# Performance work log

Hardware: AMD Instinct MI355X
Metric: run time of the kernel (lower is better)

Reference implementation:

```python
import jax, jax.numpy as jnp
import numpy as np


def setup_inputs() -> dict:
    key = jax.random.key(0)
    k1, k2, k3, k4 = jax.random.split(key, 4)
    d_in, d_out = 1024, 1024
    x = jax.random.normal(k1, (4, 2048, d_in), dtype=jnp.float32)
    # nn.Linear weights, stored as [d_in, d_out] for x @ W (torch stores transpose)
    s = 1.0 / np.sqrt(d_in)
    Wq = jax.random.normal(k2, (d_in, d_out), dtype=jnp.float32) * s
    Wk = jax.random.normal(k3, (d_in, d_out), dtype=jnp.float32) * s
    Wv = jax.random.normal(k4, (d_in, d_out), dtype=jnp.float32) * s
    return {"x": x, "Wq": Wq, "Wk": Wk, "Wv": Wv}


def reference(x, Wq, Wk, Wv):
    # x: [b, s, d_in]; projections (no bias)
    q = jnp.einsum('bsi,io->bso', x, Wq)
    k = jnp.einsum('bsi,io->bso', x, Wk)
    v = jnp.einsum('bsi,io->bso', x, Wv)
    d_out = k.shape[-1]
    scores = jnp.einsum('bqd,bkd->bqk', q, k) / jnp.sqrt(jnp.float32(d_out))
    seq_len = x.shape[1]
    causal = jnp.tril(jnp.ones((seq_len, seq_len), dtype=bool))  # [s, s]
    scores = jnp.where(causal[None, :, :], scores, -jnp.inf)
    weights = jax.nn.softmax(scores, axis=-1)
    return jnp.einsum('bqk,bkd->bqd', weights, v)
```

## Files before the change

### kernel.cpp

```cpp
#include <hip/hip_runtime.h>

typedef __attribute__((ext_vector_type(8))) short bf16x8;
typedef __attribute__((ext_vector_type(4))) float f32x4;
typedef unsigned int u32;

__device__ __forceinline__ unsigned short f2bf(float f) {
  union { float f; unsigned int u; } a; a.f = f;
  unsigned int u = a.u;
  u += 0x7FFFu + ((u >> 16) & 1u);
  return (unsigned short)(u >> 16);
}

__device__ __forceinline__ void gload16(const unsigned short* g, unsigned short* l) {
  __builtin_amdgcn_global_load_lds((const __attribute__((address_space(1))) u32*)g,
                                   (__attribute__((address_space(3))) u32*)l, 16, 0, 0);
}

#define TM 128
#define TN 128
#define BK 64

template<int MODE>
__global__ __launch_bounds__(256, 4)
void gemm_bt(const unsigned short* __restrict__ A,
             const unsigned short* __restrict__ Bm,
             float* __restrict__ Cf,
             float* __restrict__ Cf2,
             unsigned short* __restrict__ Cb,
             int K, long aBatch, long bBatch, long cBatch, float scale)
{
  int z = blockIdx.z;
  A  += (long)z * aBatch;
  Bm += (long)z * bBatch;
  if (MODE == 2) { Cb += (long)z * cBatch; Cf += (long)z * 2048; }
  if (MODE == 3) { Cf += (long)z * cBatch; Cf2 += (long)z * 2048; }

  int bm, bn;
  if (MODE == 2) {
    int f = blockIdx.x;
    int r = (int)((sqrtf((float)(8 * f + 1)) - 1.0f) * 0.5f);
    while ((r + 1) * (r + 2) / 2 <= f) r++;
    while (r * (r + 1) / 2 > f) r--;
    bm = r * TM;
    bn = (f - r * (r + 1) / 2) * TN;
  } else if (MODE == 3) {
    bm = (15 - blockIdx.y) * TM;
    bn = blockIdx.x * TN;
  } else {
    bm = blockIdx.y * TM;
    bn = blockIdx.x * TN;
  }
  int Keff = (MODE == 3) ? (bm + TM) : K;

  __shared__ __align__(16) unsigned short As[TM * BK];
  __shared__ __align__(16) unsigned short Bs[TN * BK];

  int tid  = threadIdx.x;
  int wave = tid >> 6, lane = tid & 63;
  int wm = (wave >> 1) * 64, wn = (wave & 1) * 64;
  int quad = lane >> 4, l16 = lane & 15;

  int r8 = lane >> 3;
  int c  = (lane & 7) ^ r8;
  int rs = wave * 32 + r8;
  const unsigned short* Ag = A  + (long)(bm + rs) * K + c * 8;
  const unsigned short* Bg = Bm + (long)(bn + rs) * K + c * 8;
  unsigned short* Al = &As[(wave * 32) * BK];
  unsigned short* Bl = &Bs[(wave * 32) * BK];

  f32x4 acc[4][4] = {};

  for (int k0 = 0; k0 < Keff; k0 += BK) {
#pragma unroll
    for (int g = 0; g < 4; g++) {
      gload16(Ag + k0 + (long)g * 8 * K, Al + g * 8 * BK);
      gload16(Bg + k0 + (long)g * 8 * K, Bl + g * 8 * BK);
    }
    __syncthreads();

#pragma unroll
    for (int h = 0; h < 2; h++) {
      bf16x8 af[4], bfr[4];
#pragma unroll
      for (int i = 0; i < 4; i++)
        af[i]  = *(const bf16x8*)&As[(wm + i * 16 + l16) * BK + (((quad + 4 * h) ^ (l16 & 7)) * 8)];
#pragma unroll
      for (int j = 0; j < 4; j++)
        bfr[j] = *(const bf16x8*)&Bs[(wn + j * 16 + l16) * BK + (((quad + 4 * h) ^ (l16 & 7)) * 8)];
#pragma unroll
      for (int i = 0; i < 4; i++)
#pragma unroll
        for (int j = 0; j < 4; j++)
          acc[i][j] = __builtin_amdgcn_mfma_f32_16x16x32_bf16(af[i], bfr[j], acc[i][j], 0, 0, 0);
    }
    __syncthreads();
  }

#pragma unroll
  for (int i = 0; i < 4; i++) {
    int grow0 = bm + wm + i * 16 + quad * 4;
    if (MODE == 2) {
#pragma unroll
      for (int r = 0; r < 4; r++) {
        int grow = grow0 + r;
        float rowpart = 0.f;
#pragma unroll
        for (int j = 0; j < 4; j++) {
          int gcol = bn + wn + j * 16 + l16;
          float e = (gcol <= grow) ? __expf(acc[i][j][r] * scale) : 0.f;
          rowpart += e;
          Cb[(long)grow * 2048 + gcol] = f2bf(e);
        }
        rowpart += __shfl_xor(rowpart, 1);
        rowpart += __shfl_xor(rowpart, 2);
        rowpart += __shfl_xor(rowpart, 4);
        rowpart += __shfl_xor(rowpart, 8);
        if (l16 == 0) atomicAdd(&Cf[grow], rowpart);
      }
    } else if (MODE == 3) {
      float rinv[4];
#pragma unroll
      for (int r = 0; r < 4; r++) rinv[r] = 1.0f / Cf2[grow0 + r];
#pragma unroll
      for (int j = 0; j < 4; j++) {
        int gcol = bn + wn + j * 16 + l16;
#pragma unroll
        for (int r = 0; r < 4; r++)
          Cf[(long)(grow0 + r) * 1024 + gcol] = acc[i][j][r] * rinv[r];
      }
    } else {
#pragma unroll
      for (int j = 0; j < 4; j++) {
        int gcol = bn + wn + j * 16 + l16;
        int which = gcol >> 10;
        int col = gcol & 1023;
        if (which < 2) {
          unsigned short* dst = Cb + (long)which * 8192 * 1024;
#pragma unroll
          for (int r = 0; r < 4; r++)
            dst[(long)(grow0 + r) * 1024 + col] = f2bf(acc[i][j][r]);
        } else {
          unsigned short* Vt = Cb + (long)2 * 8192 * 1024;
          int bb = grow0 >> 11, s = grow0 & 2047;
          ushort4 pk;
          pk.x = f2bf(acc[i][j][0]); pk.y = f2bf(acc[i][j][1]);
          pk.z = f2bf(acc[i][j][2]); pk.w = f2bf(acc[i][j][3]);
          *(ushort4*)(Vt + ((long)bb * 1024 + col) * 2048 + s) = pk;
        }
      }
    }
  }
}

__global__ __launch_bounds__(256)
void cvt_bf16(const float* __restrict__ in, unsigned short* __restrict__ out, long n)
{
  long i = ((long)blockIdx.x * 256 + threadIdx.x) * 4;
  if (i >= n) return;
  float4 v = *(const float4*)(in + i);
  ushort4 o;
  o.x = f2bf(v.x); o.y = f2bf(v.y); o.z = f2bf(v.z); o.w = f2bf(v.w);
  *(ushort4*)(out + i) = o;
}

__global__ __launch_bounds__(256)
void zero_rsum(float* __restrict__ rsum)
{
  long i = ((long)blockIdx.x * 256 + threadIdx.x) * 4;
  float4 zz = {0.f, 0.f, 0.f, 0.f};
  *(float4*)(rsum + i) = zz;
}

__global__ __launch_bounds__(256)
void trans_cvt(const float* __restrict__ W0, const float* __restrict__ W1, const float* __restrict__ W2,
               unsigned short* __restrict__ T0, unsigned short* __restrict__ T1, unsigned short* __restrict__ T2)
{
  int z = blockIdx.z;
  const float* W   = (z == 0) ? W0 : (z == 1) ? W1 : W2;
  unsigned short* T = (z == 0) ? T0 : (z == 1) ? T1 : T2;
  __shared__ float tile[32][33];
  int kb = blockIdx.x * 32, nb = blockIdx.y * 32;
  int tx = threadIdx.x & 31, ty = threadIdx.x >> 5;
  for (int r = ty; r < 32; r += 8)
    tile[r][tx] = W[(long)(kb + r) * 1024 + nb + tx];
  __syncthreads();
  for (int r = ty; r < 32; r += 8)
    T[(long)(nb + r) * 1024 + kb + tx] = f2bf(tile[tx][r]);
}

extern "C" void kernel_launch(void* const* d_in, const int* in_sizes, int n_in,
                              void* d_out, int out_size, void* d_ws, size_t ws_size,
                              hipStream_t stream) {
  const float* x  = (const float*)d_in[0];
  const float* Wq = (const float*)d_in[1];
  const float* Wk = (const float*)d_in[2];
  const float* Wv = (const float*)d_in[3];
  float* out = (float*)d_out;

  unsigned short* Xb  = (unsigned short*)d_ws;
  unsigned short* WqT = Xb  + (long)8192 * 1024;
  unsigned short* Q   = WqT + (long)3072 * 1024;
  unsigned short* Kb  = Q   + (long)8192 * 1024;
  unsigned short* Vt  = Kb  + (long)8192 * 1024;
  unsigned short* E   = Vt  + (long)8192 * 1024;
  float* rsum         = (float*)(E + (long)4 * 2048 * 2048);
  unsigned short* WkT = WqT + (long)1024 * 1024;
  unsigned short* WvT = WkT + (long)1024 * 1024;

  cvt_bf16<<<8192, 256, 0, stream>>>(x, Xb, (long)8388608);
  trans_cvt<<<dim3(32, 32, 3), 256, 0, stream>>>(Wq, Wk, Wv, WqT, WkT, WvT);
  zero_rsum<<<8, 256, 0, stream>>>(rsum);

  gemm_bt<0><<<dim3(24, 64, 1), 256, 0, stream>>>(Xb, WqT, nullptr, nullptr, Q,
      1024, 0, 0, 0, 1.f);

  gemm_bt<2><<<dim3(136, 1, 4), 256, 0, stream>>>(Q, Kb, rsum, nullptr, E, 1024,
      (long)2048 * 1024, (long)2048 * 1024, (long)2048 * 2048, 0.03125f);

  gemm_bt<3><<<dim3(8, 16, 4), 256, 0, stream>>>(E, Vt, out, rsum, nullptr, 2048,
      (long)2048 * 2048, (long)1024 * 2048, (long)2048 * 1024, 1.f);
}
```

Baseline: 239.0 us.

## Use 128x64 tiles for attention GEMMs, pair causal row tiles, fuse prep kernels

```diff
diff --git a/kernel.cpp b/kernel.cpp
--- a/kernel.cpp
+++ b/kernel.cpp
@@ -16,8 +16,6 @@
                                    (__attribute__((address_space(3))) u32*)l, 16, 0, 0);
 }
 
-#define TM 128
-#define TN 128
 #define BK 64
 
 template<int MODE>
@@ -29,123 +27,134 @@
              unsigned short* __restrict__ Cb,
              int K, long aBatch, long bBatch, long cBatch, float scale)
 {
+  constexpr int NI    = (MODE == 0) ? 4 : 2;
+  constexpr int TNc   = (MODE == 0) ? 128 : 64;
+  constexpr int BROWS = (MODE == 0) ? 32 : 16;
+  constexpr int BG    = (MODE == 0) ? 4 : 2;
+
   int z = blockIdx.z;
   A  += (long)z * aBatch;
   Bm += (long)z * bBatch;
   if (MODE == 2) { Cb += (long)z * cBatch; Cf += (long)z * 2048; }
   if (MODE == 3) { Cf += (long)z * cBatch; Cf2 += (long)z * 2048; }
 
-  int bm, bn;
+  int bm0 = 0, bn, p = 0;
   if (MODE == 2) {
     int f = blockIdx.x;
-    int r = (int)((sqrtf((float)(8 * f + 1)) - 1.0f) * 0.5f);
-    while ((r + 1) * (r + 2) / 2 <= f) r++;
-    while (r * (r + 1) / 2 > f) r--;
-    bm = r * TM;
-    bn = (f - r * (r + 1) / 2) * TN;
+    int r = (int)((sqrtf((float)(4 * f + 1)) - 1.0f) * 0.5f);
+    while ((r + 1) * (r + 2) <= f) r++;
+    while (r * (r + 1) > f) r--;
+    bm0 = r * 128;
+    bn  = (f - r * (r + 1)) * 64;
   } else if (MODE == 3) {
-    bm = (15 - blockIdx.y) * TM;
-    bn = blockIdx.x * TN;
+    p  = blockIdx.y;
+    bn = blockIdx.x * 64;
   } else {
-    bm = blockIdx.y * TM;
-    bn = blockIdx.x * TN;
+    bm0 = blockIdx.y * 128;
+    bn  = blockIdx.x * 128;
   }
-  int Keff = (MODE == 3) ? (bm + TM) : K;
-
-  __shared__ __align__(16) unsigned short As[TM * BK];
-  __shared__ __align__(16) unsigned short Bs[TN * BK];
+
+  __shared__ __align__(16) unsigned short As[128 * BK];
+  __shared__ __align__(16) unsigned short Bs[TNc * BK];
 
   int tid  = threadIdx.x;
   int wave = tid >> 6, lane = tid & 63;
-  int wm = (wave >> 1) * 64, wn = (wave & 1) * 64;
+  int wm = (MODE == 0) ? (wave >> 1) * 64 : wave * 32;
+  int wn = (MODE == 0) ? (wave & 1) * 64 : 0;
   int quad = lane >> 4, l16 = lane & 15;
 
   int r8 = lane >> 3;
   int c  = (lane & 7) ^ r8;
-  int rs = wave * 32 + r8;
-  const unsigned short* Ag = A  + (long)(bm + rs) * K + c * 8;
-  const unsigned short* Bg = Bm + (long)(bn + rs) * K + c * 8;
+  const unsigned short* Bg = Bm + (long)(bn + wave * BROWS + r8) * K + c * 8;
   unsigned short* Al = &As[(wave * 32) * BK];
-  unsigned short* Bl = &Bs[(wave * 32) * BK];
-
-  f32x4 acc[4][4] = {};
-
-  for (int k0 = 0; k0 < Keff; k0 += BK) {
-#pragma unroll
-    for (int g = 0; g < 4; g++) {
-      gload16(Ag + k0 + (long)g * 8 * K, Al + g * 8 * BK);
-      gload16(Bg + k0 + (long)g * 8 * K, Bl + g * 8 * BK);
+  unsigned short* Bl = &Bs[(wave * BROWS) * BK];
+
+  const int nseg = (MODE == 3) ? 2 : 1;
+  for (int seg = 0; seg < nseg; seg++) {
+    int bm   = (MODE == 3) ? ((seg == 0) ? (15 - p) * 128 : p * 128) : bm0;
+    int Keff = (MODE == 3) ? ((seg == 0) ? 128 * (16 - p) : 128 * (p + 1)) : K;
+    const unsigned short* Ag = A + (long)(bm + wave * 32 + r8) * K + c * 8;
+
+    f32x4 acc[NI][4] = {};
+
+    for (int k0 = 0; k0 < Keff; k0 += BK) {
+#pragma unroll
+      for (int g = 0; g < 4; g++)
+        gload16(Ag + k0 + (long)g * 8 * K, Al + g * 8 * BK);
+#pragma unroll
+      for (int g = 0; g < BG; g++)
+        gload16(Bg + k0 + (long)g * 8 * K, Bl + g * 8 * BK);
+      __syncthreads();
+
+#pragma unroll
+      for (int h = 0; h < 2; h++) {
+        bf16x8 af[NI], bfr[4];
+#pragma unroll
+        for (int i = 0; i < NI; i++)
+          af[i]  = *(const bf16x8*)&As[(wm + i * 16 + l16) * BK + (((quad + 4 * h) ^ (l16 & 7)) * 8)];
+#pragma unroll
+        for (int j = 0; j < 4; j++)
+          bfr[j] = *(const bf16x8*)&Bs[(wn + j * 16 + l16) * BK + (((quad + 4 * h) ^ (l16 & 7)) * 8)];
+#pragma unroll
+        for (int i = 0; i < NI; i++)
+#pragma unroll
+          for (int j = 0; j < 4; j++)
+            acc[i][j] = __builtin_amdgcn_mfma_f32_16x16x32_bf16(af[i], bfr[j], acc[i][j], 0, 0, 0);
+      }
+      __syncthreads();
     }
-    __syncthreads();
-
-#pragma unroll
-    for (int h = 0; h < 2; h++) {
-      bf16x8 af[4], bfr[4];
-#pragma unroll
-      for (int i = 0; i < 4; i++)
-        af[i]  = *(const bf16x8*)&As[(wm + i * 16 + l16) * BK + (((quad + 4 * h) ^ (l16 & 7)) * 8)];
-#pragma unroll
-      for (int j = 0; j < 4; j++)
-        bfr[j] = *(const bf16x8*)&Bs[(wn + j * 16 + l16) * BK + (((quad + 4 * h) ^ (l16 & 7)) * 8)];
-#pragma unroll
-      for (int i = 0; i < 4; i++)
-#pragma unroll
-        for (int j = 0; j < 4; j++)
-          acc[i][j] = __builtin_amdgcn_mfma_f32_16x16x32_bf16(af[i], bfr[j], acc[i][j], 0, 0, 0);
-    }
-    __syncthreads();
-  }
-
-#pragma unroll
-  for (int i = 0; i < 4; i++) {
-    int grow0 = bm + wm + i * 16 + quad * 4;
-    if (MODE == 2) {
-#pragma unroll
-      for (int r = 0; r < 4; r++) {
-        int grow = grow0 + r;
-        float rowpart = 0.f;
+
+#pragma unroll
+    for (int i = 0; i < NI; i++) {
+      int grow0 = bm + wm + i * 16 + quad * 4;
+      if (MODE == 2) {
+#pragma unroll
+        for (int r = 0; r < 4; r++) {
+          int grow = grow0 + r;
+          float rowpart = 0.f;
+#pragma unroll
+          for (int j = 0; j < 4; j++) {
+            int gcol = bn + j * 16 + l16;
+            float e = (gcol <= grow) ? __expf(acc[i][j][r] * scale) : 0.f;
+            rowpart += e;
+            Cb[(long)grow * 2048 + gcol] = f2bf(e);
+          }
+          rowpart += __shfl_xor(rowpart, 1);
+          rowpart += __shfl_xor(rowpart, 2);
+          rowpart += __shfl_xor(rowpart, 4);
+          rowpart += __shfl_xor(rowpart, 8);
+          if (l16 == 0) atomicAdd(&Cf[grow], rowpart);
+        }
+      } else if (MODE == 3) {
+        float rinv[4];
+#pragma unroll
+        for (int r = 0; r < 4; r++) rinv[r] = 1.0f / Cf2[grow0 + r];
+#pragma unroll
+        for (int j = 0; j < 4; j++) {
+          int gcol = bn + j * 16 + l16;
+#pragma unroll
+          for (int r = 0; r < 4; r++)
+            Cf[(long)(grow0 + r) * 1024 + gcol] = acc[i][j][r] * rinv[r];
+        }
+      } else {
 #pragma unroll
         for (int j = 0; j < 4; j++) {
           int gcol = bn + wn + j * 16 + l16;
-          float e = (gcol <= grow) ? __expf(acc[i][j][r] * scale) : 0.f;
-          rowpart += e;
-          Cb[(long)grow * 2048 + gcol] = f2bf(e);
-        }
-        rowpart += __shfl_xor(rowpart, 1);
-        rowpart += __shfl_xor(rowpart, 2);
-        rowpart += __shfl_xor(rowpart, 4);
-        rowpart += __shfl_xor(rowpart, 8);
-        if (l16 == 0) atomicAdd(&Cf[grow], rowpart);
-      }
-    } else if (MODE == 3) {
-      float rinv[4];
-#pragma unroll
-      for (int r = 0; r < 4; r++) rinv[r] = 1.0f / Cf2[grow0 + r];
-#pragma unroll
-      for (int j = 0; j < 4; j++) {
-        int gcol = bn + wn + j * 16 + l16;
-#pragma unroll
-        for (int r = 0; r < 4; r++)
-          Cf[(long)(grow0 + r) * 1024 + gcol] = acc[i][j][r] * rinv[r];
-      }
-    } else {
-#pragma unroll
-      for (int j = 0; j < 4; j++) {
-        int gcol = bn + wn + j * 16 + l16;
-        int which = gcol >> 10;
-        int col = gcol & 1023;
-        if (which < 2) {
-          unsigned short* dst = Cb + (long)which * 8192 * 1024;
-#pragma unroll
-          for (int r = 0; r < 4; r++)
-            dst[(long)(grow0 + r) * 1024 + col] = f2bf(acc[i][j][r]);
-        } else {
-          unsigned short* Vt = Cb + (long)2 * 8192 * 1024;
-          int bb = grow0 >> 11, s = grow0 & 2047;
-          ushort4 pk;
-          pk.x = f2bf(acc[i][j][0]); pk.y = f2bf(acc[i][j][1]);
-          pk.z = f2bf(acc[i][j][2]); pk.w = f2bf(acc[i][j][3]);
-          *(ushort4*)(Vt + ((long)bb * 1024 + col) * 2048 + s) = pk;
+          int which = gcol >> 10;
+          int col = gcol & 1023;
+          if (which < 2) {
+            unsigned short* dst = Cb + (long)which * 8192 * 1024;
+#pragma unroll
+            for (int r = 0; r < 4; r++)
+              dst[(long)(grow0 + r) * 1024 + col] = f2bf(acc[i][j][r]);
+          } else {
+            unsigned short* Vt = Cb + (long)2 * 8192 * 1024;
+            int bb = grow0 >> 11, s = grow0 & 2047;
+            ushort4 pk;
+            pk.x = f2bf(acc[i][j][0]); pk.y = f2bf(acc[i][j][1]);
+            pk.z = f2bf(acc[i][j][2]); pk.w = f2bf(acc[i][j][3]);
+            *(ushort4*)(Vt + ((long)bb * 1024 + col) * 2048 + s) = pk;
+          }
         }
       }
     }
@@ -153,39 +162,39 @@
 }
 
 __global__ __launch_bounds__(256)
-void cvt_bf16(const float* __restrict__ in, unsigned short* __restrict__ out, long n)
+void prep(const float* __restrict__ x,
+          const float* __restrict__ W0, const float* __restrict__ W1,
+          const float* __restrict__ W2,
+          unsigned short* __restrict__ Xb,
+          unsigned short* __restrict__ T0, unsigned short* __restrict__ T1,
+          unsigned short* __restrict__ T2,
+          float* __restrict__ rsum)
 {
-  long i = ((long)blockIdx.x * 256 + threadIdx.x) * 4;
-  if (i >= n) return;
-  float4 v = *(const float4*)(in + i);
-  ushort4 o;
-  o.x = f2bf(v.x); o.y = f2bf(v.y); o.z = f2bf(v.z); o.w = f2bf(v.w);
-  *(ushort4*)(out + i) = o;
-}
-
-__global__ __launch_bounds__(256)
-void zero_rsum(float* __restrict__ rsum)
-{
-  long i = ((long)blockIdx.x * 256 + threadIdx.x) * 4;
-  float4 zz = {0.f, 0.f, 0.f, 0.f};
-  *(float4*)(rsum + i) = zz;
-}
-
-__global__ __launch_bounds__(256)
-void trans_cvt(const float* __restrict__ W0, const float* __restrict__ W1, const float* __restrict__ W2,
-               unsigned short* __restrict__ T0, unsigned short* __restrict__ T1, unsigned short* __restrict__ T2)
-{
-  int z = blockIdx.z;
-  const float* W   = (z == 0) ? W0 : (z == 1) ? W1 : W2;
-  unsigned short* T = (z == 0) ? T0 : (z == 1) ? T1 : T2;
   __shared__ float tile[32][33];
-  int kb = blockIdx.x * 32, nb = blockIdx.y * 32;
-  int tx = threadIdx.x & 31, ty = threadIdx.x >> 5;
-  for (int r = ty; r < 32; r += 8)
-    tile[r][tx] = W[(long)(kb + r) * 1024 + nb + tx];
-  __syncthreads();
-  for (int r = ty; r < 32; r += 8)
-    T[(long)(nb + r) * 1024 + kb + tx] = f2bf(tile[tx][r]);
+  int b = blockIdx.x;
+  if (b < 8192) {
+    long i = ((long)b * 256 + threadIdx.x) * 4;
+    float4 v = *(const float4*)(x + i);
+    ushort4 o;
+    o.x = f2bf(v.x); o.y = f2bf(v.y); o.z = f2bf(v.z); o.w = f2bf(v.w);
+    *(ushort4*)(Xb + i) = o;
+  } else if (b < 11264) {
+    int t = b - 8192;
+    int z = t >> 10, q = t & 1023;
+    const float* W    = (z == 0) ? W0 : (z == 1) ? W1 : W2;
+    unsigned short* T = (z == 0) ? T0 : (z == 1) ? T1 : T2;
+    int kb = (q >> 5) * 32, nb = (q & 31) * 32;
+    int tx = threadIdx.x & 31, ty = threadIdx.x >> 5;
+    for (int r = ty; r < 32; r += 8)
+      tile[r][tx] = W[(long)(kb + r) * 1024 + nb + tx];
+    __syncthreads();
+    for (int r = ty; r < 32; r += 8)
+      T[(long)(nb + r) * 1024 + kb + tx] = f2bf(tile[tx][r]);
+  } else {
+    long i = ((long)(b - 11264) * 256 + threadIdx.x) * 4;
+    float4 zz = {0.f, 0.f, 0.f, 0.f};
+    *(float4*)(rsum + i) = zz;
+  }
 }
 
 extern "C" void kernel_launch(void* const* d_in, const int* in_sizes, int n_in,
@@ -207,16 +216,14 @@
   unsigned short* WkT = WqT + (long)1024 * 1024;
   unsigned short* WvT = WkT + (long)1024 * 1024;
 
-  cvt_bf16<<<8192, 256, 0, stream>>>(x, Xb, (long)8388608);
-  trans_cvt<<<dim3(32, 32, 3), 256, 0, stream>>>(Wq, Wk, Wv, WqT, WkT, WvT);
-  zero_rsum<<<8, 256, 0, stream>>>(rsum);
+  prep<<<11272, 256, 0, stream>>>(x, Wq, Wk, Wv, Xb, WqT, WkT, WvT, rsum);
 
   gemm_bt<0><<<dim3(24, 64, 1), 256, 0, stream>>>(Xb, WqT, nullptr, nullptr, Q,
       1024, 0, 0, 0, 1.f);
 
-  gemm_bt<2><<<dim3(136, 1, 4), 256, 0, stream>>>(Q, Kb, rsum, nullptr, E, 1024,
+  gemm_bt<2><<<dim3(272, 1, 4), 256, 0, stream>>>(Q, Kb, rsum, nullptr, E, 1024,
       (long)2048 * 1024, (long)2048 * 1024, (long)2048 * 2048, 0.03125f);
 
-  gemm_bt<3><<<dim3(8, 16, 4), 256, 0, stream>>>(E, Vt, out, rsum, nullptr, 2048,
+  gemm_bt<3><<<dim3(16, 8, 4), 256, 0, stream>>>(E, Vt, out, rsum, nullptr, 2048,
       (long)2048 * 2048, (long)1024 * 2048, (long)2048 * 1024, 1.f);
 }
```

New measurement: 223.5 us. 1.07x faster.
